# Optimization experiments

Hardware: AMD Instinct MI355X
Metric: run time of the kernel (lower is better)

Reference implementation:

```python
import jax, jax.numpy as jnp
import numpy as np

EPS = 1e-12  # torch F.normalize eps
SIGMA_RBF = 1.0  # rbf bandwidth (init arg sigma=1)


def _l2norm(v, axis=-1):
    return v / jnp.maximum(jnp.linalg.norm(v, axis=axis, keepdims=True), EPS)


def setup_inputs() -> dict:
    key = jax.random.key(0)
    kx, kw, kb, ku, kc = jax.random.split(key, 5)
    B, C, E, F = 512, 100, 2048, 128
    x = jax.random.normal(kx, (B, E), dtype=jnp.float32)
    # per-class Linear weights [C, F, E] and biases [C, F] (torch Linear layout: out x in)
    bound = 1.0 / np.sqrt(E)
    W = jax.random.uniform(kw, (C, F, E), minval=-bound, maxval=bound, dtype=jnp.float32)
    b = jax.random.uniform(kb, (C, F), minval=-bound, maxval=bound, dtype=jnp.float32)
    # spectral-norm power-iteration vectors u (one per class, normalized)
    u = _l2norm(jax.random.normal(ku, (C, F), dtype=jnp.float32))
    # centroid buffer c (EMA means; randn stand-in for a trained state)
    c = jax.random.normal(kc, (C, F), dtype=jnp.float32)
    return {"x": x, "W": W, "b": b, "u": u, "c": c}


def reference(x, W, b, u, c):
    # --- spectral norm: one power-iteration step per class (torch default) ---
    v = _l2norm(jnp.einsum('cfe,cf->ce', W, u))        # v = normalize(W^T u)  [C,E]
    u2 = _l2norm(jnp.einsum('cfe,ce->cf', W, v))       # u = normalize(W v)    [C,F]
    sigma = jnp.einsum('cf,cfe,ce->c', u2, W, v)       # sigma = u^T W v       [C]
    Wn = W / sigma[:, None, None]
    # --- fused per-class linear projections: z[b,c,f] ---
    z = jnp.einsum('be,cfe->bcf', x, Wn) + b[None, :, :]
    # --- RBF to centroids: exp(-||c - z||^2 / (2 sigma^2)) ---
    dist2 = jnp.sum((c[None, :, :] - z) ** 2, axis=-1)  # [B, C]
    probs = jnp.exp(-dist2 / (2.0 * SIGMA_RBF ** 2))
    return probs
```

## Files before the change

### kernel.cpp

```cpp
#include <hip/hip_runtime.h>
#include <math.h>

#define B_ 512
#define C_ 100
#define E_ 2048
#define F_ 128

typedef _Float16 f16x8 __attribute__((ext_vector_type(8)));
typedef _Float16 f16x4 __attribute__((ext_vector_type(4)));
typedef float    f32x4 __attribute__((ext_vector_type(4)));

#define AS1q __attribute__((address_space(1)))
#define AS3q __attribute__((address_space(3)))

__device__ __forceinline__ void gl_lds16(const void* g, void* lds_base) {
    __builtin_amdgcn_global_load_lds((const AS1q void*)g, (AS3q void*)lds_base, 16, 0, 0);
}

__global__ __launch_bounds__(256)
void k_conv_x(const float* __restrict__ x, _Float16* __restrict__ xh) {
    const int row = blockIdx.x;
    const int t   = threadIdx.x;
    const float* src = x + (size_t)row * E_ + t * 8;
    float4 a = *(const float4*)(src);
    float4 b = *(const float4*)(src + 4);
    f16x8 h;
    h[0] = (_Float16)a.x; h[1] = (_Float16)a.y; h[2] = (_Float16)a.z; h[3] = (_Float16)a.w;
    h[4] = (_Float16)b.x; h[5] = (_Float16)b.y; h[6] = (_Float16)b.z; h[7] = (_Float16)b.w;
    *(f16x8*)(xh + (size_t)row * E_ + t * 8) = h;
}

__global__ __launch_bounds__(256)
void k_conv_w(const float* __restrict__ W, _Float16* __restrict__ Wh) {
    const size_t base = (size_t)blockIdx.x * 32768 + threadIdx.x * 8;
#pragma unroll
    for (int it = 0; it < 16; ++it) {
        const size_t idx = base + (size_t)it * 2048;
        float4 a = *(const float4*)(W + idx);
        float4 b = *(const float4*)(W + idx + 4);
        f16x8 h;
        h[0] = (_Float16)a.x; h[1] = (_Float16)a.y; h[2] = (_Float16)a.z; h[3] = (_Float16)a.w;
        h[4] = (_Float16)b.x; h[5] = (_Float16)b.y; h[6] = (_Float16)b.z; h[7] = (_Float16)b.w;
        *(f16x8*)(Wh + idx) = h;
    }
}

__global__ __launch_bounds__(256, 1)
void k_gramsig(const _Float16* __restrict__ Wh, const float* __restrict__ u,
               float* __restrict__ rsig) {
    const int c  = blockIdx.x;
    const int t  = threadIdx.x;
    const int w  = t >> 6;
    const int l  = t & 63;
    const int wm = w & 1, wn = w >> 1;
    const int ln = l & 15, quad = l >> 4;

    __shared__ _Float16 Ts[128 * 64];

    f32x4 acc[4][4];
#pragma unroll
    for (int mt = 0; mt < 4; ++mt)
#pragma unroll
        for (int nt = 0; nt < 4; ++nt) acc[mt][nt] = (f32x4){0.f, 0.f, 0.f, 0.f};

    const int lr = l >> 3;
    const int lg = (l & 7) ^ lr;
    const _Float16* wsrc = Wh + ((size_t)c * F_ + w * 32 + lr) * E_ + lg * 8;

    for (int k0 = 0; k0 < E_; k0 += 64) {
#pragma unroll
        for (int q = 0; q < 4; ++q)
            gl_lds16(wsrc + (size_t)q * 8 * E_ + k0, &Ts[(w * 4 + q) * 512]);
        __syncthreads();

#pragma unroll
        for (int kk = 0; kk < 64; kk += 32) {
            const int g0 = (kk >> 3) + quad;
            const int sw = (g0 ^ (ln & 7)) * 8;
            f16x8 av[4], bv[4];
#pragma unroll
            for (int mt = 0; mt < 4; ++mt)
                av[mt] = *(const f16x8*)&Ts[(wm * 64 + mt * 16 + ln) * 64 + sw];
#pragma unroll
            for (int nt = 0; nt < 4; ++nt)
                bv[nt] = *(const f16x8*)&Ts[(wn * 64 + nt * 16 + ln) * 64 + sw];
#pragma unroll
            for (int mt = 0; mt < 4; ++mt)
#pragma unroll
                for (int nt = 0; nt < 4; ++nt)
                    acc[mt][nt] = __builtin_amdgcn_mfma_f32_16x16x32_f16(
                        av[mt], bv[nt], acc[mt][nt], 0, 0, 0);
        }
        __syncthreads();
    }

    const float* uc = u + (size_t)c * F_;
    float un[4];
#pragma unroll
    for (int nt = 0; nt < 4; ++nt) un[nt] = uc[wn * 64 + nt * 16 + ln];

    float* ypart = (float*)&Ts[0];

#pragma unroll
    for (int mt = 0; mt < 4; ++mt) {
#pragma unroll
        for (int r = 0; r < 4; ++r) {
            float py = acc[mt][0][r] * un[0];
            py = fmaf(acc[mt][1][r], un[1], py);
            py = fmaf(acc[mt][2][r], un[2], py);
            py = fmaf(acc[mt][3][r], un[3], py);
            py += __shfl_xor(py, 1, 64);
            py += __shfl_xor(py, 2, 64);
            py += __shfl_xor(py, 4, 64);
            py += __shfl_xor(py, 8, 64);
            if (ln == 0) {
                int m = wm * 64 + mt * 16 + quad * 4 + r;
                ypart[m * 2 + wn] = py;
            }
        }
    }
    __syncthreads();

    __shared__ float red2[2][2];
    if (t < 128) {
        float y   = ypart[t * 2] + ypart[t * 2 + 1];
        float nvp = uc[t] * y;
        float tsp = y * y;
        for (int off = 32; off; off >>= 1) {
            nvp += __shfl_down(nvp, off, 64);
            tsp += __shfl_down(tsp, off, 64);
        }
        if (l == 0) { red2[t >> 6][0] = nvp; red2[t >> 6][1] = tsp; }
    }
    __syncthreads();
    if (t == 0) {
        float nv = red2[0][0] + red2[1][0];
        float ts = red2[0][1] + red2[1][1];
        rsig[c] = sqrtf(nv / ts);
    }
}

__global__ __launch_bounds__(128, 2)
void k_main(const _Float16* __restrict__ xh, const _Float16* __restrict__ Wh,
            const float* __restrict__ bias, const float* __restrict__ cent,
            const float* __restrict__ rsig, float* __restrict__ out) {
    const int c  = blockIdx.y;
    const int b0 = blockIdx.x * 128;
    const int t  = threadIdx.x;
    const int w  = t >> 6;
    const int l  = t & 63;
    const int ln = l & 15, quad = l >> 4;

    __shared__ _Float16 Xs[128 * 64];
    __shared__ _Float16 Ws[128 * 64];

    f32x4 acc[4][8];
#pragma unroll
    for (int mt = 0; mt < 4; ++mt)
#pragma unroll
        for (int nt = 0; nt < 8; ++nt) acc[mt][nt] = (f32x4){0.f, 0.f, 0.f, 0.f};

    const int lr = l >> 3;
    const int lg = (l & 7) ^ lr;
    const _Float16* xsrc = xh + (size_t)(b0 + w * 64 + lr) * E_ + lg * 8;
    const _Float16* wsrc = Wh + ((size_t)c * F_ + w * 64 + lr) * E_ + lg * 8;

    for (int k0 = 0; k0 < E_; k0 += 64) {
#pragma unroll
        for (int q = 0; q < 8; ++q)
            gl_lds16(xsrc + (size_t)q * 8 * E_ + k0, &Xs[(w * 8 + q) * 512]);
#pragma unroll
        for (int q = 0; q < 8; ++q)
            gl_lds16(wsrc + (size_t)q * 8 * E_ + k0, &Ws[(w * 8 + q) * 512]);
        __syncthreads();

#pragma unroll
        for (int kk = 0; kk < 64; kk += 32) {
            const int g0 = (kk >> 3) + quad;
            const int sw = (g0 ^ (ln & 7)) * 8;
            f16x8 av[4], bv[8];
#pragma unroll
            for (int mt = 0; mt < 4; ++mt)
                av[mt] = *(const f16x8*)&Xs[(w * 64 + mt * 16 + ln) * 64 + sw];
#pragma unroll
            for (int nt = 0; nt < 8; ++nt)
                bv[nt] = *(const f16x8*)&Ws[(nt * 16 + ln) * 64 + sw];
#pragma unroll
            for (int mt = 0; mt < 4; ++mt)
#pragma unroll
                for (int nt = 0; nt < 8; ++nt)
                    acc[mt][nt] = __builtin_amdgcn_mfma_f32_16x16x32_f16(
                        av[mt], bv[nt], acc[mt][nt], 0, 0, 0);
        }
        __syncthreads();
    }

    const float rsigma = rsig[c];

    float bi[8], ce[8];
#pragma unroll
    for (int nt = 0; nt < 8; ++nt) {
        int f = nt * 16 + ln;
        bi[nt] = bias[c * F_ + f];
        ce[nt] = cent[c * F_ + f];
    }

#pragma unroll
    for (int mt = 0; mt < 4; ++mt) {
#pragma unroll
        for (int r = 0; r < 4; ++r) {
            float part = 0.f;
#pragma unroll
            for (int nt = 0; nt < 8; ++nt) {
                float z = fmaf(acc[mt][nt][r], rsigma, bi[nt]);
                float d = ce[nt] - z;
                part = fmaf(d, d, part);
            }
            part += __shfl_xor(part, 1, 64);
            part += __shfl_xor(part, 2, 64);
            part += __shfl_xor(part, 4, 64);
            part += __shfl_xor(part, 8, 64);
            if (ln == 0) {
                int m = w * 64 + mt * 16 + quad * 4 + r;
                out[(size_t)(b0 + m) * C_ + c] = expf(-0.5f * part);
            }
        }
    }
}

extern "C" void kernel_launch(void* const* d_in, const int* in_sizes, int n_in,
                              void* d_out, int out_size, void* d_ws, size_t ws_size,
                              hipStream_t stream) {
    const float* x  = (const float*)d_in[0];
    const float* W  = (const float*)d_in[1];
    const float* b  = (const float*)d_in[2];
    const float* u  = (const float*)d_in[3];
    const float* cc = (const float*)d_in[4];
    float* out = (float*)d_out;

    char* ws = (char*)d_ws;
    _Float16* Wh   = (_Float16*)ws;
    _Float16* xh   = (_Float16*)(ws + (size_t)C_ * F_ * E_ * 2);
    float*    rsig = (float*)(ws + (size_t)C_ * F_ * E_ * 2 + (size_t)B_ * E_ * 2);

    k_conv_x<<<B_, 256, 0, stream>>>(x, xh);
    k_conv_w<<<800, 256, 0, stream>>>(W, Wh);
    k_gramsig<<<C_, 256, 0, stream>>>(Wh, u, rsig);

    dim3 grid(B_ / 128, C_);
    k_main<<<grid, 128, 0, stream>>>(xh, Wh, b, cc, rsig, out);
}
```

Measured before the change: 255.9 us.

## Split Gram sigma over K chunks, merge conversions, widen main kernel to 4 waves

The per-class Gram/sigma kernel now runs 8 K-chunks per class, accumulates y with atomics, and finishes in a small rsig kernel, so far more blocks run than the previous 100. The two fp32-to-fp16 conversion kernels are merged into one launch. k_main moves from 2 waves to 4 waves per 128x128 tile with a 2x2 wave split and a cross-wave LDS reduction, which raises occupancy and lowers register pressure. The cost is an extra memset and kernel launch, atomic traffic, and non-deterministic summation order.

```diff
diff --git a/kernel.cpp b/kernel.cpp
--- a/kernel.cpp
+++ b/kernel.cpp
@@ -7,7 +7,6 @@
 #define F_ 128
 
 typedef _Float16 f16x8 __attribute__((ext_vector_type(8)));
-typedef _Float16 f16x4 __attribute__((ext_vector_type(4)));
 typedef float    f32x4 __attribute__((ext_vector_type(4)));
 
 #define AS1q __attribute__((address_space(1)))
@@ -18,37 +17,29 @@
 }
 
 __global__ __launch_bounds__(256)
-void k_conv_x(const float* __restrict__ x, _Float16* __restrict__ xh) {
-    const int row = blockIdx.x;
-    const int t   = threadIdx.x;
-    const float* src = x + (size_t)row * E_ + t * 8;
-    float4 a = *(const float4*)(src);
-    float4 b = *(const float4*)(src + 4);
-    f16x8 h;
-    h[0] = (_Float16)a.x; h[1] = (_Float16)a.y; h[2] = (_Float16)a.z; h[3] = (_Float16)a.w;
-    h[4] = (_Float16)b.x; h[5] = (_Float16)b.y; h[6] = (_Float16)b.z; h[7] = (_Float16)b.w;
-    *(f16x8*)(xh + (size_t)row * E_ + t * 8) = h;
-}
-
-__global__ __launch_bounds__(256)
-void k_conv_w(const float* __restrict__ W, _Float16* __restrict__ Wh) {
-    const size_t base = (size_t)blockIdx.x * 32768 + threadIdx.x * 8;
+void k_conv(const float* __restrict__ W, _Float16* __restrict__ Wh,
+            const float* __restrict__ x, _Float16* __restrict__ xh) {
+    const int blk = blockIdx.x;
+    const float* src; _Float16* dst; size_t base;
+    if (blk < 800) { src = W; dst = Wh; base = (size_t)blk * 32768 + threadIdx.x * 8; }
+    else           { src = x; dst = xh; base = (size_t)(blk - 800) * 32768 + threadIdx.x * 8; }
 #pragma unroll
     for (int it = 0; it < 16; ++it) {
         const size_t idx = base + (size_t)it * 2048;
-        float4 a = *(const float4*)(W + idx);
-        float4 b = *(const float4*)(W + idx + 4);
+        float4 a = *(const float4*)(src + idx);
+        float4 b = *(const float4*)(src + idx + 4);
         f16x8 h;
         h[0] = (_Float16)a.x; h[1] = (_Float16)a.y; h[2] = (_Float16)a.z; h[3] = (_Float16)a.w;
         h[4] = (_Float16)b.x; h[5] = (_Float16)b.y; h[6] = (_Float16)b.z; h[7] = (_Float16)b.w;
-        *(f16x8*)(Wh + idx) = h;
-    }
-}
-
-__global__ __launch_bounds__(256, 1)
-void k_gramsig(const _Float16* __restrict__ Wh, const float* __restrict__ u,
-               float* __restrict__ rsig) {
-    const int c  = blockIdx.x;
+        *(f16x8*)(dst + idx) = h;
+    }
+}
+
+__global__ __launch_bounds__(256, 2)
+void k_gram_y(const _Float16* __restrict__ Wh, const float* __restrict__ u,
+              float* __restrict__ y) {
+    const int chunk = blockIdx.x;
+    const int c  = blockIdx.y;
     const int t  = threadIdx.x;
     const int w  = t >> 6;
     const int l  = t & 63;
@@ -66,8 +57,9 @@
     const int lr = l >> 3;
     const int lg = (l & 7) ^ lr;
     const _Float16* wsrc = Wh + ((size_t)c * F_ + w * 32 + lr) * E_ + lg * 8;
-
-    for (int k0 = 0; k0 < E_; k0 += 64) {
+    const int kbase = chunk * 256;
+
+    for (int k0 = kbase; k0 < kbase + 256; k0 += 64) {
 #pragma unroll
         for (int q = 0; q < 4; ++q)
             gl_lds16(wsrc + (size_t)q * 8 * E_ + k0, &Ts[(w * 4 + q) * 512]);
@@ -98,8 +90,6 @@
     float un[4];
 #pragma unroll
     for (int nt = 0; nt < 4; ++nt) un[nt] = uc[wn * 64 + nt * 16 + ln];
-
-    float* ypart = (float*)&Ts[0];
 
 #pragma unroll
     for (int mt = 0; mt < 4; ++mt) {
@@ -115,32 +105,29 @@
             py += __shfl_xor(py, 8, 64);
             if (ln == 0) {
                 int m = wm * 64 + mt * 16 + quad * 4 + r;
-                ypart[m * 2 + wn] = py;
+                atomicAdd(&y[(size_t)c * F_ + m], py);
             }
         }
     }
-    __syncthreads();
-
-    __shared__ float red2[2][2];
-    if (t < 128) {
-        float y   = ypart[t * 2] + ypart[t * 2 + 1];
-        float nvp = uc[t] * y;
-        float tsp = y * y;
-        for (int off = 32; off; off >>= 1) {
-            nvp += __shfl_down(nvp, off, 64);
-            tsp += __shfl_down(tsp, off, 64);
-        }
-        if (l == 0) { red2[t >> 6][0] = nvp; red2[t >> 6][1] = tsp; }
-    }
-    __syncthreads();
-    if (t == 0) {
-        float nv = red2[0][0] + red2[1][0];
-        float ts = red2[0][1] + red2[1][1];
-        rsig[c] = sqrtf(nv / ts);
-    }
-}
-
-__global__ __launch_bounds__(128, 2)
+}
+
+__global__ __launch_bounds__(64)
+void k_rsig(const float* __restrict__ u, const float* __restrict__ y,
+            float* __restrict__ rsig) {
+    const int c = blockIdx.x;
+    const int l = threadIdx.x;
+    float y0 = y[(size_t)c * F_ + l],      y1 = y[(size_t)c * F_ + 64 + l];
+    float u0 = u[(size_t)c * F_ + l],      u1 = u[(size_t)c * F_ + 64 + l];
+    float nv = u0 * y0 + u1 * y1;
+    float ts = y0 * y0 + y1 * y1;
+    for (int off = 32; off; off >>= 1) {
+        nv += __shfl_down(nv, off, 64);
+        ts += __shfl_down(ts, off, 64);
+    }
+    if (l == 0) rsig[c] = sqrtf(nv / ts);
+}
+
+__global__ __launch_bounds__(256, 2)
 void k_main(const _Float16* __restrict__ xh, const _Float16* __restrict__ Wh,
             const float* __restrict__ bias, const float* __restrict__ cent,
             const float* __restrict__ rsig, float* __restrict__ out) {
@@ -149,46 +136,47 @@
     const int t  = threadIdx.x;
     const int w  = t >> 6;
     const int l  = t & 63;
+    const int wm = w & 1, wn = w >> 1;
     const int ln = l & 15, quad = l >> 4;
 
     __shared__ _Float16 Xs[128 * 64];
     __shared__ _Float16 Ws[128 * 64];
 
-    f32x4 acc[4][8];
+    f32x4 acc[4][4];
 #pragma unroll
     for (int mt = 0; mt < 4; ++mt)
 #pragma unroll
-        for (int nt = 0; nt < 8; ++nt) acc[mt][nt] = (f32x4){0.f, 0.f, 0.f, 0.f};
+        for (int nt = 0; nt < 4; ++nt) acc[mt][nt] = (f32x4){0.f, 0.f, 0.f, 0.f};
 
     const int lr = l >> 3;
     const int lg = (l & 7) ^ lr;
-    const _Float16* xsrc = xh + (size_t)(b0 + w * 64 + lr) * E_ + lg * 8;
-    const _Float16* wsrc = Wh + ((size_t)c * F_ + w * 64 + lr) * E_ + lg * 8;
+    const _Float16* xsrc = xh + (size_t)(b0 + w * 32 + lr) * E_ + lg * 8;
+    const _Float16* wsrc = Wh + ((size_t)c * F_ + w * 32 + lr) * E_ + lg * 8;
 
     for (int k0 = 0; k0 < E_; k0 += 64) {
 #pragma unroll
-        for (int q = 0; q < 8; ++q)
-            gl_lds16(xsrc + (size_t)q * 8 * E_ + k0, &Xs[(w * 8 + q) * 512]);
-#pragma unroll
-        for (int q = 0; q < 8; ++q)
-            gl_lds16(wsrc + (size_t)q * 8 * E_ + k0, &Ws[(w * 8 + q) * 512]);
+        for (int q = 0; q < 4; ++q)
+            gl_lds16(xsrc + (size_t)q * 8 * E_ + k0, &Xs[(w * 4 + q) * 512]);
+#pragma unroll
+        for (int q = 0; q < 4; ++q)
+            gl_lds16(wsrc + (size_t)q * 8 * E_ + k0, &Ws[(w * 4 + q) * 512]);
         __syncthreads();
 
 #pragma unroll
         for (int kk = 0; kk < 64; kk += 32) {
             const int g0 = (kk >> 3) + quad;
             const int sw = (g0 ^ (ln & 7)) * 8;
-            f16x8 av[4], bv[8];
-#pragma unroll
-            for (int mt = 0; mt < 4; ++mt)
-                av[mt] = *(const f16x8*)&Xs[(w * 64 + mt * 16 + ln) * 64 + sw];
-#pragma unroll
-            for (int nt = 0; nt < 8; ++nt)
-                bv[nt] = *(const f16x8*)&Ws[(nt * 16 + ln) * 64 + sw];
-#pragma unroll
-            for (int mt = 0; mt < 4; ++mt)
-#pragma unroll
-                for (int nt = 0; nt < 8; ++nt)
+            f16x8 av[4], bv[4];
+#pragma unroll
+            for (int mt = 0; mt < 4; ++mt)
+                av[mt] = *(const f16x8*)&Xs[(wm * 64 + mt * 16 + ln) * 64 + sw];
+#pragma unroll
+            for (int nt = 0; nt < 4; ++nt)
+                bv[nt] = *(const f16x8*)&Ws[(wn * 64 + nt * 16 + ln) * 64 + sw];
+#pragma unroll
+            for (int mt = 0; mt < 4; ++mt)
+#pragma unroll
+                for (int nt = 0; nt < 4; ++nt)
                     acc[mt][nt] = __builtin_amdgcn_mfma_f32_16x16x32_f16(
                         av[mt], bv[nt], acc[mt][nt], 0, 0, 0);
         }
@@ -197,21 +185,23 @@
 
     const float rsigma = rsig[c];
 
-    float bi[8], ce[8];
-#pragma unroll
-    for (int nt = 0; nt < 8; ++nt) {
-        int f = nt * 16 + ln;
+    float bi[4], ce[4];
+#pragma unroll
+    for (int nt = 0; nt < 4; ++nt) {
+        int f = wn * 64 + nt * 16 + ln;
         bi[nt] = bias[c * F_ + f];
         ce[nt] = cent[c * F_ + f];
     }
 
+    float* red = (float*)&Xs[0];
+
 #pragma unroll
     for (int mt = 0; mt < 4; ++mt) {
 #pragma unroll
         for (int r = 0; r < 4; ++r) {
             float part = 0.f;
 #pragma unroll
-            for (int nt = 0; nt < 8; ++nt) {
+            for (int nt = 0; nt < 4; ++nt) {
                 float z = fmaf(acc[mt][nt][r], rsigma, bi[nt]);
                 float d = ce[nt] - z;
                 part = fmaf(d, d, part);
@@ -221,10 +211,15 @@
             part += __shfl_xor(part, 4, 64);
             part += __shfl_xor(part, 8, 64);
             if (ln == 0) {
-                int m = w * 64 + mt * 16 + quad * 4 + r;
-                out[(size_t)(b0 + m) * C_ + c] = expf(-0.5f * part);
+                int m = wm * 64 + mt * 16 + quad * 4 + r;
+                red[m * 2 + wn] = part;
             }
         }
+    }
+    __syncthreads();
+    if (t < 128) {
+        float d2 = red[t * 2] + red[t * 2 + 1];
+        out[(size_t)(b0 + t) * C_ + c] = expf(-0.5f * d2);
     }
 }
 
@@ -241,12 +236,17 @@
     char* ws = (char*)d_ws;
     _Float16* Wh   = (_Float16*)ws;
     _Float16* xh   = (_Float16*)(ws + (size_t)C_ * F_ * E_ * 2);
-    float*    rsig = (float*)(ws + (size_t)C_ * F_ * E_ * 2 + (size_t)B_ * E_ * 2);
-
-    k_conv_x<<<B_, 256, 0, stream>>>(x, xh);
-    k_conv_w<<<800, 256, 0, stream>>>(W, Wh);
-    k_gramsig<<<C_, 256, 0, stream>>>(Wh, u, rsig);
+    float*    yv   = (float*)(ws + (size_t)C_ * F_ * E_ * 2 + (size_t)B_ * E_ * 2);
+    float*    rsig = yv + (size_t)C_ * F_;
+
+    hipMemsetAsync(yv, 0, (size_t)C_ * F_ * sizeof(float), stream);
+
+    k_conv<<<832, 256, 0, stream>>>(W, Wh, x, xh);
+
+    dim3 ggrid(8, C_);
+    k_gram_y<<<ggrid, 256, 0, stream>>>(Wh, u, yv);
+    k_rsig<<<C_, 64, 0, stream>>>(u, yv, rsig);
 
     dim3 grid(B_ / 128, C_);
-    k_main<<<grid, 128, 0, stream>>>(xh, Wh, b, cc, rsig, out);
-}
+    k_main<<<grid, 256, 0, stream>>>(xh, Wh, b, cc, rsig, out);
+}
```

Measured after the change: 232.0 us. 1.1x faster.
